# Kernel tuning notes

Hardware: AMD Instinct MI355X
Metric: run time of the kernel (lower is better)

## Reference

```python
import jax, jax.numpy as jnp
import numpy as np

B, T = 64, 32
EMBED, HIDDEN, VOCAB = 512, 1024, 32000


def setup_inputs() -> dict:
    key = jax.random.key(0)
    ks = jax.random.split(key, 8)
    inputs = jax.random.randint(ks[0], (B, T), 0, VOCAB)
    encoder_features = jax.random.normal(ks[1], (B, EMBED), dtype=jnp.float32)
    h0 = jnp.zeros((B, HIDDEN), dtype=jnp.float32)
    c0 = jnp.zeros((B, HIDDEN), dtype=jnp.float32)
    # parameters (PyTorch LSTM layout: gates ordered i, f, g, o)
    s_e = 1.0 / np.sqrt(EMBED)
    s_h = 1.0 / np.sqrt(HIDDEN)
    embed_table = jax.random.normal(ks[2], (VOCAB, EMBED), dtype=jnp.float32)
    W_ih = jax.random.uniform(ks[3], (4 * HIDDEN, 2 * EMBED), minval=-s_h, maxval=s_h, dtype=jnp.float32)
    W_hh = jax.random.uniform(ks[4], (4 * HIDDEN, HIDDEN), minval=-s_h, maxval=s_h, dtype=jnp.float32)
    b_ih = jnp.zeros((4 * HIDDEN,), dtype=jnp.float32)
    b_hh = jnp.zeros((4 * HIDDEN,), dtype=jnp.float32)
    fc_W = jax.random.uniform(ks[5], (VOCAB, HIDDEN), minval=-s_h, maxval=s_h, dtype=jnp.float32)
    fc_b = jnp.zeros((VOCAB,), dtype=jnp.float32)
    return dict(inputs=inputs, encoder_features=encoder_features, h0=h0, c0=c0,
                embed_table=embed_table, W_ih=W_ih, W_hh=W_hh, b_ih=b_ih, b_hh=b_hh,
                fc_W=fc_W, fc_b=fc_b)


def reference(inputs, encoder_features, h0, c0, embed_table, W_ih, W_hh, b_ih, b_hh, fc_W, fc_b):
    H = h0.shape[-1]
    embeds = embed_table[inputs]                     # [B, T, E]
    # Per-step input is concat([word_t, encoder_features]); precompute x@W_ih^T
    # by splitting W_ih into word / encoder halves (encoder part is constant per step).
    E = embeds.shape[-1]
    W_word = W_ih[:, :E]                             # [4H, E]
    W_enc = W_ih[:, E:]                              # [4H, E]
    enc_proj = encoder_features @ W_enc.T + b_ih + b_hh   # [B, 4H]
    x_proj = jnp.einsum('bte,ge->btg', embeds, W_word) + enc_proj[:, None, :]  # [B, T, 4H]

    def cell(carry, xp_t):
        h, c = carry
        z = xp_t + h @ W_hh.T                        # [B, 4H]
        i, f, g, o = jnp.split(z, 4, axis=-1)
        c = jax.nn.sigmoid(f) * c + jax.nn.sigmoid(i) * jnp.tanh(g)
        h = jax.nn.sigmoid(o) * jnp.tanh(c)
        return (h, c), h

    (hn, cn), hs = jax.lax.scan(cell, (h0, c0), jnp.swapaxes(x_proj, 0, 1))  # hs: [T, B, H]
    hs = jnp.swapaxes(hs, 0, 1)                      # [B, T, H]
    logits = jnp.einsum('bth,vh->btv', hs, fc_W) + fc_b  # [B, T, V]
    return logits, hn, cn
```

## Files before the change

### kernel.cpp

```cpp
#include <hip/hip_runtime.h>
#include <hip/hip_bf16.h>
#include <cstdint>


typedef __bf16 bf16x8 __attribute__((ext_vector_type(8)));
typedef __bf16 bf16x4 __attribute__((ext_vector_type(4)));
typedef float  f32x4  __attribute__((ext_vector_type(4)));

__device__ __forceinline__ void gload_lds16(const void* g, void* l) {
  __builtin_amdgcn_global_load_lds(
      (const __attribute__((address_space(1))) void*)g,
      (__attribute__((address_space(3))) void*)l, 16, 0, 0);
}

__device__ __forceinline__ float sigf(float x) {
  x = fminf(fmaxf(x, -30.f), 30.f);
  return 1.f / (1.f + __expf(-x));
}
__device__ __forceinline__ float tanhf_(float x) {
  x = fminf(fmaxf(x, -15.f), 15.f);
  float e = __expf(2.f * x);
  return (e - 1.f) / (e + 1.f);
}


__global__ __launch_bounds__(256) void cast_bf16_kernel(
    const float* __restrict__ s, __bf16* __restrict__ d, long n4) {
  long i = (long)blockIdx.x * 256 + threadIdx.x;
  long stride = (long)gridDim.x * 256;
  for (; i < n4; i += stride) {
    float4 v = ((const float4*)s)[i];
    bf16x4 o = {(__bf16)v.x, (__bf16)v.y, (__bf16)v.z, (__bf16)v.w};
    *(bf16x4*)(d + i * 4) = o;
  }
}

__global__ __launch_bounds__(256) void bias_sum_kernel(
    const float* __restrict__ a, const float* __restrict__ b,
    float* __restrict__ o) {
  int i = blockIdx.x * 256 + threadIdx.x;
  o[i] = a[i] + b[i];
}

__global__ __launch_bounds__(256) void init_hc_kernel(
    const float* __restrict__ h0, const float* __restrict__ c0,
    __bf16* __restrict__ hbuf, float* __restrict__ c_st) {
  int i = blockIdx.x * 256 + threadIdx.x;
  hbuf[i] = (__bf16)h0[i];
  c_st[i] = c0[i];
}

__global__ __launch_bounds__(256) void gather_xin_kernel(
    const int* __restrict__ inp, const float* __restrict__ emb,
    const float* __restrict__ enc, __bf16* __restrict__ xin) {
  int m = blockIdx.x;
  int tid = threadIdx.x;
  int idx = inp[m];
  int b = m >> 5;
  int col = tid * 4;
  const float* src = (col < 512) ? emb + (size_t)idx * 512 + col
                                 : enc + (size_t)b * 512 + (col - 512);
  float4 v = *(const float4*)src;
  bf16x4 o = {(__bf16)v.x, (__bf16)v.y, (__bf16)v.z, (__bf16)v.w};
  *(bf16x4*)(xin + (size_t)m * 1024 + col) = o;
}

__global__ __launch_bounds__(256) void gemm_bt(
    const __bf16* __restrict__ A, const __bf16* __restrict__ B,
    float* __restrict__ C, const float* __restrict__ colBias,
    int M, int N, int K) {
  __shared__ __bf16 As[128][64];
  __shared__ __bf16 Bs[128][64];
  const int tid = threadIdx.x;
  const int w = tid >> 6, l = tid & 63;
  const int m0 = blockIdx.y * 128, n0 = blockIdx.x * 128;
  const int wm = (w >> 1) * 64, wn = (w & 1) * 64;
  const int lr = l >> 3;
  const int lc = (l & 7) * 8;
  const int fr = l & 15;
  const int fk = (l >> 4) * 8;
  f32x4 acc[4][4] = {};

  for (int kt = 0; kt < K; kt += 64) {
    __syncthreads();
#pragma unroll
    for (int i = 0; i < 4; ++i) {
      int row = i * 32 + w * 8;
      gload_lds16(A + (size_t)(m0 + row + lr) * K + kt + lc, &As[row][0]);
      gload_lds16(B + (size_t)(n0 + row + lr) * K + kt + lc, &Bs[row][0]);
    }
    __syncthreads();
#pragma unroll
    for (int ks = 0; ks < 2; ++ks) {
      bf16x8 a[4], b[4];
#pragma unroll
      for (int mi = 0; mi < 4; ++mi)
        a[mi] = *(const bf16x8*)&As[wm + mi * 16 + fr][ks * 32 + fk];
#pragma unroll
      for (int ni = 0; ni < 4; ++ni)
        b[ni] = *(const bf16x8*)&Bs[wn + ni * 16 + fr][ks * 32 + fk];
#pragma unroll
      for (int mi = 0; mi < 4; ++mi)
#pragma unroll
        for (int ni = 0; ni < 4; ++ni)
          acc[mi][ni] = __builtin_amdgcn_mfma_f32_16x16x32_bf16(
              a[mi], b[ni], acc[mi][ni], 0, 0, 0);
    }
  }

  const int col = l & 15, rowb = (l >> 4) * 4;
#pragma unroll
  for (int mi = 0; mi < 4; ++mi)
#pragma unroll
    for (int ni = 0; ni < 4; ++ni) {
      int n = n0 + wn + ni * 16 + col;
      float bias = colBias ? colBias[n] : 0.f;
#pragma unroll
      for (int r = 0; r < 4; ++r) {
        int m = m0 + wm + mi * 16 + rowb + r;
        C[(size_t)m * N + n] = acc[mi][ni][r] + bias;
      }
    }
}

__global__ __launch_bounds__(256) void lstm_step(
    const __bf16* __restrict__ hin, const __bf16* __restrict__ Whh,
    const float* __restrict__ xproj, float* __restrict__ c_st,
    __bf16* __restrict__ hout, __bf16* __restrict__ hs,
    float* __restrict__ hn, float* __restrict__ cn, int t) {
  __shared__ __bf16 As[64][64];
  __shared__ __bf16 Bs[4][16][64];
  const int tid = threadIdx.x, w = tid >> 6, l = tid & 63;
  const int j0 = blockIdx.x * 16;
  const int lr = l >> 3, lc = (l & 7) * 8;
  const int fr = l & 15, fk = (l >> 4) * 8;
  f32x4 acc[4] = {};

  for (int kt = 0; kt < 1024; kt += 64) {
    __syncthreads();
#pragma unroll
    for (int i = 0; i < 2; ++i) {
      int row = w * 16 + i * 8;
      gload_lds16(hin + (size_t)(row + lr) * 1024 + kt + lc, &As[row][0]);
      int frow = row + lr;
      int gate = frow >> 4, jr = frow & 15;
      gload_lds16(Whh + (size_t)(gate * 1024 + j0 + jr) * 1024 + kt + lc,
                  (__bf16*)Bs + (size_t)row * 64);
    }
    __syncthreads();
#pragma unroll
    for (int ks = 0; ks < 2; ++ks) {
      bf16x8 a = *(const bf16x8*)&As[w * 16 + fr][ks * 32 + fk];
#pragma unroll
      for (int g = 0; g < 4; ++g) {
        bf16x8 b = *(const bf16x8*)&Bs[g][fr][ks * 32 + fk];
        acc[g] = __builtin_amdgcn_mfma_f32_16x16x32_bf16(a, b, acc[g], 0, 0, 0);
      }
    }
  }

  const int col = l & 15, rowb = (l >> 4) * 4;
  const int j = j0 + col;
#pragma unroll
  for (int r = 0; r < 4; ++r) {
    int b = w * 16 + rowb + r;
    size_t xbase = ((size_t)b * 32 + t) * 4096 + j;
    float zi = acc[0][r] + xproj[xbase];
    float zf = acc[1][r] + xproj[xbase + 1024];
    float zg = acc[2][r] + xproj[xbase + 2048];
    float zo = acc[3][r] + xproj[xbase + 3072];
    float ii = sigf(zi), ff = sigf(zf), gg = tanhf_(zg), oo = sigf(zo);
    size_t hc = (size_t)b * 1024 + j;
    float cv = ff * c_st[hc] + ii * gg;
    float hv = oo * tanhf_(cv);
    c_st[hc] = cv;
    __bf16 hb = (__bf16)hv;
    hout[hc] = hb;
    hs[((size_t)b * 32 + t) * 1024 + j] = hb;
    if (t == 31) { hn[hc] = hv; cn[hc] = cv; }
  }
}


extern "C" void kernel_launch(void* const* d_in, const int* in_sizes, int n_in,
                              void* d_out, int out_size, void* d_ws,
                              size_t ws_size, hipStream_t stream) {
  const int*   inp = (const int*)d_in[0];
  const float* enc = (const float*)d_in[1];
  const float* h0  = (const float*)d_in[2];
  const float* c0  = (const float*)d_in[3];
  const float* emb = (const float*)d_in[4];
  const float* Wih = (const float*)d_in[5];
  const float* Whh = (const float*)d_in[6];
  const float* bih = (const float*)d_in[7];
  const float* bhh = (const float*)d_in[8];
  const float* fcW = (const float*)d_in[9];
  const float* fcb = (const float*)d_in[10];

  float* out    = (float*)d_out;
  float* logits = out;
  float* hn     = out + 65536000LL;
  float* cn     = hn + 65536;

  char* p = (char*)d_ws;
  __bf16* wih_bf = (__bf16*)p; p += 8388608;
  __bf16* whh_bf = (__bf16*)p; p += 8388608;
  __bf16* fcw_bf = (__bf16*)p; p += 65536000;
  float*  bsum   = (float*)p;  p += 16384;
  __bf16* xin    = (__bf16*)p; p += 4194304;
  float*  xproj  = (float*)p;  p += 33554432;
  __bf16* hbuf0  = (__bf16*)p; p += 131072;
  __bf16* hbuf1  = (__bf16*)p; p += 131072;
  float*  c_st   = (float*)p;  p += 262144;
  __bf16* hs     = (__bf16*)p; p += 4194304;

  cast_bf16_kernel<<<1024, 256, 0, stream>>>(Wih, wih_bf, 1048576);
  cast_bf16_kernel<<<1024, 256, 0, stream>>>(Whh, whh_bf, 1048576);
  cast_bf16_kernel<<<2048, 256, 0, stream>>>(fcW, fcw_bf, 8192000);
  bias_sum_kernel<<<16, 256, 0, stream>>>(bih, bhh, bsum);
  init_hc_kernel<<<256, 256, 0, stream>>>(h0, c0, hbuf0, c_st);
  gather_xin_kernel<<<2048, 256, 0, stream>>>(inp, emb, enc, xin);

  gemm_bt<<<dim3(32, 16), 256, 0, stream>>>(xin, wih_bf, xproj, bsum,
                                            2048, 4096, 1024);

  for (int t = 0; t < 32; ++t) {
    const __bf16* hi = (t & 1) ? hbuf1 : hbuf0;
    __bf16*       ho = (t & 1) ? hbuf0 : hbuf1;
    lstm_step<<<64, 256, 0, stream>>>(hi, whh_bf, xproj, c_st, ho, hs, hn, cn, t);
  }

  gemm_bt<<<dim3(250, 16), 256, 0, stream>>>(hs, fcw_bf, logits, fcb,
                                             2048, 32000, 1024);
}
```

Before: 1.140 ms.

## Remap GEMM workgroups across XCDs and stage full W_hh slice in swizzled LDS

The GEMM now remaps workgroup IDs so consecutive tiles land on the same XCD, and walks M fastest so tiles sharing a B column tile run together for better L2 reuse. The launch grid is transposed to match. The LSTM step kernel loads its whole 64x1024 W_hh slice into LDS once, using an XOR swizzle to avoid bank conflicts, and reads the hidden-state A operand straight from global memory, removing 16 rounds of barrier-synchronised tile loads. The kernel now uses 128KB of LDS, which limits each CU to one block, and the direct global reads of h may add latency.

```diff
diff --git a/kernel.cpp b/kernel.cpp
--- a/kernel.cpp
+++ b/kernel.cpp
@@ -73,7 +73,12 @@
   __shared__ __bf16 Bs[128][64];
   const int tid = threadIdx.x;
   const int w = tid >> 6, l = tid & 63;
-  const int m0 = blockIdx.y * 128, n0 = blockIdx.x * 128;
+  const int nwg = gridDim.x * gridDim.y;
+  const int orig = blockIdx.y * gridDim.x + blockIdx.x;
+  const int q = nwg >> 3;
+  const int wid = (orig & 7) * q + (orig >> 3);
+  const int m0 = (wid & 15) << 7;
+  const int n0 = (wid >> 4) << 7;
   const int wm = (w >> 1) * 64, wn = (w & 1) * 64;
   const int lr = l >> 3;
   const int lc = (l & 7) * 8;
@@ -128,34 +133,37 @@
     const float* __restrict__ xproj, float* __restrict__ c_st,
     __bf16* __restrict__ hout, __bf16* __restrict__ hs,
     float* __restrict__ hn, float* __restrict__ cn, int t) {
-  __shared__ __bf16 As[64][64];
-  __shared__ __bf16 Bs[4][16][64];
+  __shared__ alignas(16) __bf16 Bsw[4][16][1024];
   const int tid = threadIdx.x, w = tid >> 6, l = tid & 63;
   const int j0 = blockIdx.x * 16;
-  const int lr = l >> 3, lc = (l & 7) * 8;
-  const int fr = l & 15, fk = (l >> 4) * 8;
+  const int fr = l & 15;
+  const int fk = (l >> 4) * 8;
+
+  char* ldsb = (char*)&Bsw[0][0][0];
+#pragma unroll
+  for (int it = 0; it < 32; ++it) {
+    int o = it * 4096 + tid * 16;
+    int row = o >> 11;
+    int colb = o & 2047;
+    int g = row >> 4, jj = row & 15;
+    bf16x8 v = *(const bf16x8*)((const char*)Whh +
+                 ((size_t)(g << 10) + j0 + jj) * 2048 + colb);
+    *(bf16x8*)(ldsb + (row << 11) + (colb ^ ((row & 7) << 4))) = v;
+  }
+  __syncthreads();
+
+  const __bf16* aptr = hin + (size_t)(w * 16 + fr) * 1024 + fk;
+  const int xv = (fr & 7) << 4;
   f32x4 acc[4] = {};
-
-  for (int kt = 0; kt < 1024; kt += 64) {
-    __syncthreads();
-#pragma unroll
-    for (int i = 0; i < 2; ++i) {
-      int row = w * 16 + i * 8;
-      gload_lds16(hin + (size_t)(row + lr) * 1024 + kt + lc, &As[row][0]);
-      int frow = row + lr;
-      int gate = frow >> 4, jr = frow & 15;
-      gload_lds16(Whh + (size_t)(gate * 1024 + j0 + jr) * 1024 + kt + lc,
-                  (__bf16*)Bs + (size_t)row * 64);
-    }
-    __syncthreads();
-#pragma unroll
-    for (int ks = 0; ks < 2; ++ks) {
-      bf16x8 a = *(const bf16x8*)&As[w * 16 + fr][ks * 32 + fk];
-#pragma unroll
-      for (int g = 0; g < 4; ++g) {
-        bf16x8 b = *(const bf16x8*)&Bs[g][fr][ks * 32 + fk];
-        acc[g] = __builtin_amdgcn_mfma_f32_16x16x32_bf16(a, b, acc[g], 0, 0, 0);
-      }
+#pragma unroll 8
+  for (int ks = 0; ks < 32; ++ks) {
+    bf16x8 a = *(const bf16x8*)(aptr + ks * 32);
+    int cb = ks * 64 + ((l >> 4) << 4);
+#pragma unroll
+    for (int g = 0; g < 4; ++g) {
+      int rb = ((g << 4) + fr) << 11;
+      bf16x8 b = *(const bf16x8*)(ldsb + rb + (cb ^ xv));
+      acc[g] = __builtin_amdgcn_mfma_f32_16x16x32_bf16(a, b, acc[g], 0, 0, 0);
     }
   }
 
@@ -221,7 +229,7 @@
   init_hc_kernel<<<256, 256, 0, stream>>>(h0, c0, hbuf0, c_st);
   gather_xin_kernel<<<2048, 256, 0, stream>>>(inp, emb, enc, xin);
 
-  gemm_bt<<<dim3(32, 16), 256, 0, stream>>>(xin, wih_bf, xproj, bsum,
+  gemm_bt<<<dim3(16, 32), 256, 0, stream>>>(xin, wih_bf, xproj, bsum,
                                             2048, 4096, 1024);
 
   for (int t = 0; t < 32; ++t) {
@@ -230,6 +238,6 @@
     lstm_step<<<64, 256, 0, stream>>>(hi, whh_bf, xproj, c_st, ho, hs, hn, cn, t);
   }
 
-  gemm_bt<<<dim3(250, 16), 256, 0, stream>>>(hs, fcw_bf, logits, fcb,
+  gemm_bt<<<dim3(16, 250), 256, 0, stream>>>(hs, fcw_bf, logits, fcb,
                                              2048, 32000, 1024);
 }
```

New measurement: 1.067 ms. 6.4% less time.
